# Kernel tuning notes

Hardware: AMD Instinct MI355X
Metric: run time of the kernel (lower is better)

Reference implementation:

```python
import jax, jax.numpy as jnp
import numpy as np

D = 256        # controller_lstm_size
BR = 8         # child_branch_num
UNITS = 12     # child_unit_num
TEMP = 5.0
TANHC = 1.1
MAXA = UNITS + 2   # max number of anchors
NEG = -1e9


def setup_inputs() -> dict:
    key = jax.random.key(0)
    ks = jax.random.split(key, 9)
    u = lambda k, s: jax.random.uniform(k, s, jnp.float32, -0.1, 0.1)
    # b_soft: zeros with first two entries = 10, excluded from uniform init
    b_soft = jnp.zeros((BR,), jnp.float32).at[:2].set(10.0)
    return {
        "encoder": u(ks[0], (BR + 1, D)),   # nn.Embedding(branch_num+1, D)
        "W_ih": u(ks[1], (4 * D, D)),       # LSTMCell weight_ih (i,f,g,o)
        "W_hh": u(ks[2], (4 * D, D)),
        "b_ih": u(ks[3], (4 * D,)),
        "b_hh": u(ks[4], (4 * D,)),
        "w_soft": u(ks[5], (BR, D)),
        "b_soft": b_soft,
        "w_attn_1": u(ks[6], (D, D)),
        "w_attn_2": u(ks[7], (D, D)),
        "v_attn": u(ks[8], (D,)),
    }


def _sample(key, logits):
    """Categorical sample + NLL(cross_entropy) + entropy term (batch-1)."""
    idx = jax.random.categorical(key, jax.lax.stop_gradient(logits))
    logp = jax.nn.log_softmax(logits)
    ent = -jnp.sum(jax.nn.softmax(logits) * logp)
    return idx, -logp[idx], ent


def _run_sampler(p, key, c0, h0, use_bias):
    b_no_learn = jnp.asarray([0.25, 0.25] + [-0.25] * (BR - 2), jnp.float32)

    def lstm(x, h, c):
        g = x @ p["W_ih"].T + p["b_ih"] + h @ p["W_hh"].T + p["b_hh"]
        i, f, gc, o = jnp.split(g, 4, axis=-1)
        c2 = jax.nn.sigmoid(f) * c + jax.nn.sigmoid(i) * jnp.tanh(gc)
        return jax.nn.sigmoid(o) * jnp.tanh(c2), c2

    anchors = jnp.zeros((MAXA, D), jnp.float32)
    anchors_w1 = jnp.zeros((MAXA, D), jnp.float32)
    h, c = h0, c0
    x = p["encoder"][0]
    for i in range(2):  # two seed units, anchors stay zero
        h, c = lstm(x, h, c)
        anchors_w1 = anchors_w1.at[i].set(p["w_attn_1"] @ h)

    def step(carry, unit_id):
        h, c, x, anchors, anchors_w1, key, lp, ent = carry
        mask = jnp.arange(MAXA) < unit_id
        idxs, ops = [], []
        for _ in range(2):  # sample two input indices via attention
            h, c = lstm(x, h, c)
            q = jnp.tanh(anchors_w1 + p["w_attn_2"] @ h)     # [MAXA, D]
            logits = q @ p["v_attn"]                          # [MAXA]
            logits = TANHC * jnp.tanh(logits / TEMP)
            logits = jnp.where(mask, logits, NEG)
            key, sub = jax.random.split(key)
            idx, nll, e = _sample(sub, logits)
            lp = lp + nll
            ent = ent + jax.lax.stop_gradient(e)
            x = anchors[idx]
            idxs.append(idx)
        for _ in range(2):  # sample two ops
            h, c = lstm(x, h, c)
            logits = p["w_soft"] @ h + p["b_soft"]
            logits = TANHC * jnp.tanh(logits / TEMP)
            if use_bias:
                logits = logits + b_no_learn
            key, sub = jax.random.split(key)
            op, nll, e = _sample(sub, logits)
            lp = lp + nll
            ent = ent + jax.lax.stop_gradient(e)
            x = p["encoder"][op + 1]
            ops.append(op)
        h, c = lstm(x, h, c)  # final step adds a new anchor
        anchors = anchors.at[unit_id].set(h)
        anchors_w1 = anchors_w1.at[unit_id].set(p["w_attn_1"] @ h)
        x = p["encoder"][0]
        out = jnp.stack([idxs[0], ops[0], idxs[1], ops[1]])  # [idx1,op1,idx2,op2]
        return (h, c, x, anchors, anchors_w1, key, lp, ent), out

    z = jnp.float32(0.0)
    init = (h, c, x, anchors, anchors_w1, key, z, z)
    (h, c, *_rest, lp, ent), arcs = jax.lax.scan(
        step, init, jnp.arange(2, UNITS + 2))
    return arcs.reshape(-1), ent, lp, c, h


def reference(encoder, W_ih, W_hh, b_ih, b_hh, w_soft, b_soft,
              w_attn_1, w_attn_2, v_attn):
    p = {"encoder": encoder, "W_ih": W_ih, "W_hh": W_hh, "b_ih": b_ih,
         "b_hh": b_hh, "w_soft": w_soft, "b_soft": b_soft,
         "w_attn_1": w_attn_1, "w_attn_2": w_attn_2, "v_attn": v_attn}
    k1, k2 = jax.random.split(jax.random.key(123))
    z = jnp.zeros((D,), jnp.float32)
    arc1, e1, l1, c, h = _run_sampler(p, k1, z, z, use_bias=True)
    arc2, e2, l2, _, _ = _run_sampler(p, k2, c, h, use_bias=False)
    return arc1, arc2, l1 + l2, e1 + e2
```

## Files before the change

### kernel.cpp

```cpp
#include <hip/hip_runtime.h>
#include <cstdint>

#define D     256
#define NB    32
#define TPB   256
#define HS    8
#define NROW  32
#define MAXA  14
#define UNITS 12
#define NEGV  (-1e9f)

__device__ unsigned long long g_Hq[D];
__device__ unsigned long long g_PartQ[NB*16];

__global__ void init_kernel() {
  int i = threadIdx.x;
  if (i < D) g_Hq[i] = 0ull;
  if (i < NB * 16) g_PartQ[i] = 0ull;
}

__device__ __forceinline__ void qstore(unsigned long long* p, unsigned gen,
                                       float v) {
  unsigned long long q =
      ((unsigned long long)gen << 32) | (unsigned long long)__float_as_uint(v);
  __hip_atomic_store(p, q, __ATOMIC_RELAXED, __HIP_MEMORY_SCOPE_AGENT);
}

__device__ __forceinline__ float qpoll(unsigned long long* p, unsigned gen) {
  unsigned long long q;
  long spins = 0;
  for (;;) {
    q = __hip_atomic_load(p, __ATOMIC_RELAXED, __HIP_MEMORY_SCOPE_AGENT);
    if ((unsigned)(q >> 32) == gen) break;
    __builtin_amdgcn_s_sleep(2);
    if (++spins > 50000000L) break;
  }
  return __uint_as_float((unsigned)q);
}

__device__ __forceinline__ uint32_t rotl32(uint32_t v, uint32_t n) {
  return (v << n) | (v >> (32u - n));
}

__device__ uint2 tf2x32(uint2 k, uint32_t x0, uint32_t x1) {
  uint32_t ks0 = k.x, ks1 = k.y, ks2 = 0x1BD11BDAu ^ ks0 ^ ks1;
  x0 += ks0; x1 += ks1;
#define TF4(a,b,c,d) \
  x0 += x1; x1 = rotl32(x1,(a)); x1 ^= x0; \
  x0 += x1; x1 = rotl32(x1,(b)); x1 ^= x0; \
  x0 += x1; x1 = rotl32(x1,(c)); x1 ^= x0; \
  x0 += x1; x1 = rotl32(x1,(d)); x1 ^= x0;
  TF4(13,15,26,6)  x0 += ks1; x1 += ks2 + 1u;
  TF4(17,29,16,24) x0 += ks2; x1 += ks0 + 2u;
  TF4(13,15,26,6)  x0 += ks0; x1 += ks1 + 3u;
  TF4(17,29,16,24) x0 += ks1; x1 += ks2 + 4u;
  TF4(13,15,26,6)  x0 += ks2; x1 += ks0 + 5u;
#undef TF4
  return make_uint2(x0, x1);
}

__device__ __forceinline__ float gumbelf(uint32_t bits) {
  float f = __uint_as_float((bits >> 9) | 0x3f800000u) - 1.0f;
  const float tiny = 1.17549435082228751e-38f;
  float u = fmaxf(tiny, f);
  return -logf(-logf(u));
}

__device__ __forceinline__ float sigm(float x) {
  return 0.5f + 0.5f * tanhf(0.5f * x);
}

__global__ void __launch_bounds__(TPB) ENAScontroller_21706764714567_kernel(
    const float* __restrict__ enc,   const float* __restrict__ Wih,
    const float* __restrict__ Whh,   const float* __restrict__ bih,
    const float* __restrict__ bhh,   const float* __restrict__ wsoft,
    const float* __restrict__ bsoft, const float* __restrict__ wa1,
    const float* __restrict__ wa2,   const float* __restrict__ vattn,
    float* __restrict__ out)
{
  const int b    = blockIdx.x;
  const int t    = threadIdx.x;
  const int lane = t & 63;
  const int wv_  = t >> 6;

  unsigned hgen = 0;
  unsigned pgen = 0;

  __shared__ float4 sWhh4[64 * NROW];
  __shared__ float4 sWa1p[64 * HS];
  __shared__ float4 sWa2p[64 * HS];
  __shared__ __align__(16) float s_h[D];
  __shared__ float s_part[TPB];
  __shared__ float s_pp[NB * 16];
  __shared__ float s_eW[9][NROW];
  __shared__ float s_aW[MAXA][NROW];
  __shared__ float s_aw1[MAXA][HS];
  __shared__ float s_t2[HS];
  __shared__ float s_vs[HS];
  __shared__ float s_c[HS];
  __shared__ float s_bc[NROW];
  __shared__ float s_bsoft[HS];
  __shared__ float s_log[16];
  __shared__ float s_z[16];
  __shared__ uint2 s_pair[2];
  __shared__ uint2 s_key;
  __shared__ int   s_sel;
  __shared__ float s_lp, s_ent;

  for (int idx = t; idx < 64 * NROW; idx += TPB) {
    int kk = idx >> 5, j = idx & 31;
    int grow = (j >> 3) * D + b * HS + (j & 7);
    sWhh4[idx] = *(const float4*)&Whh[grow * D + kk * 4];
  }
  for (int idx = t; idx < 64 * HS; idx += TPB) {
    int kk = idx >> 3, j = idx & 7;
    sWa1p[idx] = *(const float4*)&wa1[(b * HS + j) * D + kk * 4];
    sWa2p[idx] = *(const float4*)&wa2[(b * HS + j) * D + kk * 4];
  }
  if (t < NROW) {
    int grow = (t >> 3) * D + b * HS + (t & 7);
    s_bc[t] = bih[grow] + bhh[grow];
  }
  if (t < HS) {
    s_vs[t] = vattn[b * HS + t];
    s_bsoft[t] = bsoft[t];
    s_c[t] = 0.f;
  }
  s_h[t] = 0.f;
  if (t == 0) { s_lp = 0.f; s_ent = 0.f; }
  if (t < 2) s_pair[t] = tf2x32(make_uint2(0u, 123u), 0u, (uint32_t)t);
  __syncthreads();
  const uint2 key1 = s_pair[0];
  const uint2 key2 = s_pair[1];

  for (int m = 0; m < 8; ++m) {
    int j = wv_ * 8 + m;
    int grow = wv_ * D + b * HS + m;
    float4 wrow = *(const float4*)&Wih[grow * D + lane * 4];
    for (int r = 0; r < 9; ++r) {
      float4 ev = *(const float4*)&enc[r * D + lane * 4];
      float x = wrow.x * ev.x + wrow.y * ev.y + wrow.z * ev.z + wrow.w * ev.w;
      #pragma unroll
      for (int s = 32; s; s >>= 1) x += __shfl_xor(x, s);
      if (lane == 0) s_eW[r][j] = x;
    }
  }
  __syncthreads();

  auto LSTM = [&](const float* xd) {
    {
      int j = t & 31, p = t >> 5;
      const float4* hp = (const float4*)s_h;
      float acc = 0.f;
      #pragma unroll
      for (int q = 0; q < 8; ++q) {
        int kk = p * 8 + q;
        float4 wvv = sWhh4[kk * 32 + j];
        float4 hv  = hp[kk];
        acc += wvv.x * hv.x + wvv.y * hv.y + wvv.z * hv.z + wvv.w * hv.w;
      }
      s_part[t] = acc;
    }
    __syncthreads();
    ++hgen;
    if (t < HS) {
      float gg[4];
      #pragma unroll
      for (int q = 0; q < 4; ++q) {
        int j = q * 8 + t;
        float s = s_bc[j] + xd[j];
        #pragma unroll
        for (int p = 0; p < 8; ++p) s += s_part[p * 32 + j];
        gg[q] = s;
      }
      float c2 = sigm(gg[1]) * s_c[t] + sigm(gg[0]) * tanhf(gg[2]);
      float hn = sigm(gg[3]) * tanhf(c2);
      s_c[t] = c2;
      qstore(&g_Hq[b * HS + t], hgen, hn);
    }
    float hv = qpoll(&g_Hq[t], hgen);
    s_h[t] = hv;
    __syncthreads();
  };

  auto DOT8 = [&](const float4* M, float* dst) {
    if (t < 64) {
      int j = t & 7, p = t >> 3;
      const float4* hp = (const float4*)s_h;
      float acc = 0.f;
      #pragma unroll
      for (int q = 0; q < 8; ++q) {
        int kk = p * 8 + q;
        float4 m4 = M[kk * 8 + j];
        float4 hv = hp[kk];
        acc += m4.x * hv.x + m4.y * hv.y + m4.z * hv.z + m4.w * hv.w;
      }
      s_part[t] = acc;
    }
    __syncthreads();
    if (t < 8) {
      float s = 0.f;
      #pragma unroll
      for (int p = 0; p < 8; ++p) s += s_part[p * 8 + t];
      dst[t] = s;
    }
    __syncthreads();
  };

  auto AWC = [&](int slot) {
    const float4* hp = (const float4*)s_h;
    for (int m = 0; m < 8; ++m) {
      int j = wv_ * 8 + m;
      int grow = wv_ * D + b * HS + m;
      float4 wrow = *(const float4*)&Wih[grow * D + lane * 4];
      float4 hv = hp[lane];
      float x = wrow.x * hv.x + wrow.y * hv.y + wrow.z * hv.z + wrow.w * hv.w;
      #pragma unroll
      for (int s = 32; s; s >>= 1) x += __shfl_xor(x, s);
      if (lane == 0) s_aW[slot][j] = x;
    }
    __syncthreads();
  };

  auto ATTN = [&]() {
    DOT8(sWa2p, s_t2);
    ++pgen;
    if (t < MAXA) {
      float pa = 0.f;
      #pragma unroll
      for (int d2 = 0; d2 < HS; ++d2)
        pa += tanhf(s_aw1[t][d2] + s_t2[d2]) * s_vs[d2];
      qstore(&g_PartQ[b * 16 + t], pgen, pa);
    }
    #pragma unroll
    for (int slot = t; slot < NB * 16; slot += TPB) {
      if ((slot & 15) < MAXA) s_pp[slot] = qpoll(&g_PartQ[slot], pgen);
    }
    __syncthreads();
  };

  auto ALOGITS = [&](int u) {
    if (t < MAXA) {
      float l = 0.f;
      #pragma unroll
      for (int bb = 0; bb < NB; ++bb) l += s_pp[bb * 16 + t];
      l = 1.1f * tanhf(l / 5.0f);
      s_log[t] = (t < u) ? l : NEGV;
    }
    __syncthreads();
  };

  auto OLOGITS = [&](bool useBias) {
    if (t < 64) {
      int j = t & 7, p = t >> 3;
      const float4* hp = (const float4*)s_h;
      float acc = 0.f;
      #pragma unroll
      for (int q = 0; q < 8; ++q) {
        int kk = p * 8 + q;
        float4 m4 = *(const float4*)&wsoft[j * D + kk * 4];
        float4 hv = hp[kk];
        acc += m4.x * hv.x + m4.y * hv.y + m4.z * hv.z + m4.w * hv.w;
      }
      s_part[t] = acc;
    }
    __syncthreads();
    if (t < 8) {
      float s = 0.f;
      #pragma unroll
      for (int p = 0; p < 8; ++p) s += s_part[p * 8 + t];
      float l = s + s_bsoft[t];
      l = 1.1f * tanhf(l / 5.0f);
      if (useBias) l += (t < 2 ? 0.25f : -0.25f);
      s_log[t] = l;
    }
    __syncthreads();
  };

  auto SAMPLE = [&](int N) -> int {
    if (t < 2) s_pair[t] = tf2x32(s_key, 0u, (uint32_t)t);
    __syncthreads();
    uint2 sub = s_pair[1];
    if (t == 0) s_key = s_pair[0];
    if (t < N) {
      uint2 e = tf2x32(sub, 0u, (uint32_t)t);
      s_z[t] = s_log[t] + gumbelf(e.x ^ e.y);
    }
    __syncthreads();
    if (t == 0) {
      int bi = 0; float bz = s_z[0];
      for (int a = 1; a < N; ++a) if (s_z[a] > bz) { bz = s_z[a]; bi = a; }
      float m = s_log[0];
      for (int a = 1; a < N; ++a) m = fmaxf(m, s_log[a]);
      float ssum = 0.f, sdl = 0.f;
      for (int a = 0; a < N; ++a) {
        float d2 = s_log[a] - m;
        float e2 = expf(d2);
        ssum += e2; sdl += e2 * d2;
      }
      float ls = logf(ssum);
      s_lp  += -(s_log[bi] - m - ls);
      s_ent += ls - sdl / ssum;
      s_sel = bi;
    }
    __syncthreads();
    return s_sel;
  };

  for (int smp = 0; smp < 2; ++smp) {
    for (int idx = t; idx < MAXA * NROW; idx += TPB) (&s_aW[0][0])[idx]  = 0.f;
    for (int idx = t; idx < MAXA * HS;   idx += TPB) (&s_aw1[0][0])[idx] = 0.f;
    if (t == 0) s_key = (smp == 0) ? key1 : key2;
    __syncthreads();

    for (int sd = 0; sd < 2; ++sd) {
      if (sd == 1) DOT8(sWa1p, s_aw1[0]);
      LSTM(s_eW[0]);
    }

    bool useBias = (smp == 0);
    for (int u = 2; u < 2 + UNITS; ++u) {
      DOT8(sWa1p, s_aw1[u - 1]);
      if (u > 2) AWC(u - 1);
      LSTM(s_eW[0]);

      ATTN(); ALOGITS(u);
      int i1 = SAMPLE(MAXA);
      LSTM(s_aW[i1]);

      ATTN(); ALOGITS(u);
      int i2 = SAMPLE(MAXA);
      LSTM(s_aW[i2]);

      OLOGITS(useBias);
      int o1 = SAMPLE(8);
      LSTM(s_eW[o1 + 1]);

      OLOGITS(useBias);
      int o2 = SAMPLE(8);
      LSTM(s_eW[o2 + 1]);

      if (b == 0 && t == 0) {
        int base = smp * 48 + (u - 2) * 4;
        out[base + 0] = (float)i1;
        out[base + 1] = (float)o1;
        out[base + 2] = (float)i2;
        out[base + 3] = (float)o2;
      }
    }
  }
  if (b == 0 && t == 0) {
    out[96] = s_lp;
    out[97] = s_ent;
  }
}

extern "C" __attribute__((visibility("default")))
void kernel_launch(void* const* d_in, const int* in_sizes, int n_in,
                   void* d_out, int out_size, void* d_ws, size_t ws_size,
                   hipStream_t stream) {
  const float* enc   = (const float*)d_in[0];
  const float* Wih   = (const float*)d_in[1];
  const float* Whh   = (const float*)d_in[2];
  const float* bih   = (const float*)d_in[3];
  const float* bhh   = (const float*)d_in[4];
  const float* wsoft = (const float*)d_in[5];
  const float* bsoft = (const float*)d_in[6];
  const float* wa1   = (const float*)d_in[7];
  const float* wa2   = (const float*)d_in[8];
  const float* vattn = (const float*)d_in[9];
  float* out = (float*)d_out;

  init_kernel<<<dim3(1), dim3(512), 0, stream>>>();
  ENAScontroller_21706764714567_kernel<<<dim3(NB), dim3(TPB), 0, stream>>>(
      enc, Wih, Whh, bih, bhh, wsoft, bsoft, wa1, wa2, vattn, out);
}
```

Measured before the change: 622.1 us.

## Compute attention redundantly per block to drop cross-block partial exchange

Every block now computes the full 256-wide w_attn_1/w_attn_2 matvecs and the attention logits itself, reading the weights from global memory. This removes the second inter-block polling exchange (g_PartQ) on each attention step. The LSTM is split into pre/post halves so the w_attn_1 anchor matvec overlaps the wait for the h broadcast, and g_Hq is double-buffered by generation parity. The cost is redundant global-memory matvec work in every block, plus a shorter sleep and a lower timeout in the poll loop.

```diff
diff --git a/kernel.cpp b/kernel.cpp
--- a/kernel.cpp
+++ b/kernel.cpp
@@ -10,13 +10,11 @@
 #define UNITS 12
 #define NEGV  (-1e9f)
 
-__device__ unsigned long long g_Hq[D];
-__device__ unsigned long long g_PartQ[NB*16];
+__device__ unsigned long long g_Hq[2 * D];
 
 __global__ void init_kernel() {
   int i = threadIdx.x;
-  if (i < D) g_Hq[i] = 0ull;
-  if (i < NB * 16) g_PartQ[i] = 0ull;
+  if (i < 2 * D) g_Hq[i] = 0ull;
 }
 
 __device__ __forceinline__ void qstore(unsigned long long* p, unsigned gen,
@@ -32,8 +30,8 @@
   for (;;) {
     q = __hip_atomic_load(p, __ATOMIC_RELAXED, __HIP_MEMORY_SCOPE_AGENT);
     if ((unsigned)(q >> 32) == gen) break;
-    __builtin_amdgcn_s_sleep(2);
-    if (++spins > 50000000L) break;
+    __builtin_amdgcn_s_sleep(1);
+    if (++spins > 20000000L) break;
   }
   return __uint_as_float((unsigned)q);
 }
@@ -84,22 +82,19 @@
   const int wv_  = t >> 6;
 
   unsigned hgen = 0;
-  unsigned pgen = 0;
 
   __shared__ float4 sWhh4[64 * NROW];
-  __shared__ float4 sWa1p[64 * HS];
-  __shared__ float4 sWa2p[64 * HS];
   __shared__ __align__(16) float s_h[D];
   __shared__ float s_part[TPB];
-  __shared__ float s_pp[NB * 16];
   __shared__ float s_eW[9][NROW];
   __shared__ float s_aW[MAXA][NROW];
-  __shared__ float s_aw1[MAXA][HS];
-  __shared__ float s_t2[HS];
-  __shared__ float s_vs[HS];
+  __shared__ float s_aw1[MAXA][D];
+  __shared__ float s_t2f[D];
+  __shared__ float s_v[D];
+  __shared__ float s_red2[MAXA][32];
   __shared__ float s_c[HS];
   __shared__ float s_bc[NROW];
-  __shared__ float s_bsoft[HS];
+  __shared__ float s_bsoft[8];
   __shared__ float s_log[16];
   __shared__ float s_z[16];
   __shared__ uint2 s_pair[2];
@@ -112,20 +107,13 @@
     int grow = (j >> 3) * D + b * HS + (j & 7);
     sWhh4[idx] = *(const float4*)&Whh[grow * D + kk * 4];
   }
-  for (int idx = t; idx < 64 * HS; idx += TPB) {
-    int kk = idx >> 3, j = idx & 7;
-    sWa1p[idx] = *(const float4*)&wa1[(b * HS + j) * D + kk * 4];
-    sWa2p[idx] = *(const float4*)&wa2[(b * HS + j) * D + kk * 4];
-  }
   if (t < NROW) {
     int grow = (t >> 3) * D + b * HS + (t & 7);
     s_bc[t] = bih[grow] + bhh[grow];
   }
-  if (t < HS) {
-    s_vs[t] = vattn[b * HS + t];
-    s_bsoft[t] = bsoft[t];
-    s_c[t] = 0.f;
-  }
+  s_v[t] = vattn[t];
+  if (t < 8) s_bsoft[t] = bsoft[t];
+  if (t < HS) s_c[t] = 0.f;
   s_h[t] = 0.f;
   if (t == 0) { s_lp = 0.f; s_ent = 0.f; }
   if (t < 2) s_pair[t] = tf2x32(make_uint2(0u, 123u), 0u, (uint32_t)t);
@@ -147,7 +135,7 @@
   }
   __syncthreads();
 
-  auto LSTM = [&](const float* xd) {
+  auto LSTM_PRE = [&](const float* xd) {
     {
       int j = t & 31, p = t >> 5;
       const float4* hp = (const float4*)s_h;
@@ -176,34 +164,35 @@
       float c2 = sigm(gg[1]) * s_c[t] + sigm(gg[0]) * tanhf(gg[2]);
       float hn = sigm(gg[3]) * tanhf(c2);
       s_c[t] = c2;
-      qstore(&g_Hq[b * HS + t], hgen, hn);
-    }
-    float hv = qpoll(&g_Hq[t], hgen);
+      qstore(&g_Hq[(hgen & 1) * D + b * HS + t], hgen, hn);
+    }
+  };
+
+  auto LSTM_POST = [&]() {
+    __syncthreads();
+    float hv = qpoll(&g_Hq[(hgen & 1) * D + t], hgen);
     s_h[t] = hv;
     __syncthreads();
   };
 
-  auto DOT8 = [&](const float4* M, float* dst) {
-    if (t < 64) {
-      int j = t & 7, p = t >> 3;
-      const float4* hp = (const float4*)s_h;
-      float acc = 0.f;
+  auto DOTFULL = [&](const float* __restrict__ W, float* dst) {
+    const float4* W4 = (const float4*)W;
+    const float4* hp = (const float4*)s_h;
+    int j = t;
+    float acc = 0.f;
+    #pragma unroll
+    for (int p = 0; p < 8; ++p) {
+      float pp = 0.f;
       #pragma unroll
       for (int q = 0; q < 8; ++q) {
         int kk = p * 8 + q;
-        float4 m4 = M[kk * 8 + j];
+        float4 m4 = W4[j * 64 + kk];
         float4 hv = hp[kk];
-        acc += m4.x * hv.x + m4.y * hv.y + m4.z * hv.z + m4.w * hv.w;
-      }
-      s_part[t] = acc;
-    }
-    __syncthreads();
-    if (t < 8) {
-      float s = 0.f;
-      #pragma unroll
-      for (int p = 0; p < 8; ++p) s += s_part[p * 8 + t];
-      dst[t] = s;
-    }
+        pp += m4.x * hv.x + m4.y * hv.y + m4.z * hv.z + m4.w * hv.w;
+      }
+      acc += pp;
+    }
+    dst[j] = acc;
     __syncthreads();
   };
 
@@ -222,19 +211,17 @@
     __syncthreads();
   };
 
-  auto ATTN = [&]() {
-    DOT8(sWa2p, s_t2);
-    ++pgen;
-    if (t < MAXA) {
+  auto ATTNL = [&]() {
+    DOTFULL(wa2, s_t2f);
+    for (int idx = t; idx < MAXA * 32; idx += TPB) {
+      int a = idx >> 5, bb = idx & 31;
       float pa = 0.f;
       #pragma unroll
-      for (int d2 = 0; d2 < HS; ++d2)
-        pa += tanhf(s_aw1[t][d2] + s_t2[d2]) * s_vs[d2];
-      qstore(&g_PartQ[b * 16 + t], pgen, pa);
-    }
-    #pragma unroll
-    for (int slot = t; slot < NB * 16; slot += TPB) {
-      if ((slot & 15) < MAXA) s_pp[slot] = qpoll(&g_PartQ[slot], pgen);
+      for (int d2 = 0; d2 < 8; ++d2) {
+        int d = bb * 8 + d2;
+        pa += tanhf(s_aw1[a][d] + s_t2f[d]) * s_v[d];
+      }
+      s_red2[a][bb] = pa;
     }
     __syncthreads();
   };
@@ -243,7 +230,7 @@
     if (t < MAXA) {
       float l = 0.f;
       #pragma unroll
-      for (int bb = 0; bb < NB; ++bb) l += s_pp[bb * 16 + t];
+      for (int bb = 0; bb < NB; ++bb) l += s_red2[t][bb];
       l = 1.1f * tanhf(l / 5.0f);
       s_log[t] = (t < u) ? l : NEGV;
     }
@@ -309,36 +296,38 @@
 
   for (int smp = 0; smp < 2; ++smp) {
     for (int idx = t; idx < MAXA * NROW; idx += TPB) (&s_aW[0][0])[idx]  = 0.f;
-    for (int idx = t; idx < MAXA * HS;   idx += TPB) (&s_aw1[0][0])[idx] = 0.f;
+    for (int idx = t; idx < MAXA * D;    idx += TPB) (&s_aw1[0][0])[idx] = 0.f;
     if (t == 0) s_key = (smp == 0) ? key1 : key2;
     __syncthreads();
 
-    for (int sd = 0; sd < 2; ++sd) {
-      if (sd == 1) DOT8(sWa1p, s_aw1[0]);
-      LSTM(s_eW[0]);
-    }
+    LSTM_PRE(s_eW[0]);
+    LSTM_POST();
+    LSTM_PRE(s_eW[0]);
+    DOTFULL(wa1, s_aw1[0]);
+    LSTM_POST();
 
     bool useBias = (smp == 0);
     for (int u = 2; u < 2 + UNITS; ++u) {
-      DOT8(sWa1p, s_aw1[u - 1]);
+      LSTM_PRE(s_eW[0]);
+      DOTFULL(wa1, s_aw1[u - 1]);
       if (u > 2) AWC(u - 1);
-      LSTM(s_eW[0]);
-
-      ATTN(); ALOGITS(u);
+      LSTM_POST();
+
+      ATTNL(); ALOGITS(u);
       int i1 = SAMPLE(MAXA);
-      LSTM(s_aW[i1]);
-
-      ATTN(); ALOGITS(u);
+      LSTM_PRE(s_aW[i1]); LSTM_POST();
+
+      ATTNL(); ALOGITS(u);
       int i2 = SAMPLE(MAXA);
-      LSTM(s_aW[i2]);
+      LSTM_PRE(s_aW[i2]); LSTM_POST();
 
       OLOGITS(useBias);
       int o1 = SAMPLE(8);
-      LSTM(s_eW[o1 + 1]);
+      LSTM_PRE(s_eW[o1 + 1]); LSTM_POST();
 
       OLOGITS(useBias);
       int o2 = SAMPLE(8);
-      LSTM(s_eW[o2 + 1]);
+      LSTM_PRE(s_eW[o2 + 1]); LSTM_POST();
 
       if (b == 0 && t == 0) {
         int base = smp * 48 + (u - 2) * 4;
```

After: 877.5 us. 1.41x slower.

## Double-buffer cross-block exchange slots and overlap LSTM h exchange with DOT8

Applied to the files above, without the earlier changes.

Splits the LSTM step into a compute/publish phase and a poll/gather phase, so the attention-key DOT8 and AWC work run while other blocks' hidden states are still arriving. The global h and attention-partial exchange buffers are double-buffered by generation parity to avoid overwrite races when blocks run ahead. Polling is now done by 64 threads each fetching several slots, and the sleep interval is shortened. This adds extra block barriers and concentrates the polling latency on fewer threads.

```diff
diff --git a/kernel.cpp b/kernel.cpp
--- a/kernel.cpp
+++ b/kernel.cpp
@@ -10,13 +10,13 @@
 #define UNITS 12
 #define NEGV  (-1e9f)
 
-__device__ unsigned long long g_Hq[D];
-__device__ unsigned long long g_PartQ[NB*16];
+__device__ unsigned long long g_Hq[2 * D];
+__device__ unsigned long long g_PartQ[2 * NB*16];
 
 __global__ void init_kernel() {
   int i = threadIdx.x;
-  if (i < D) g_Hq[i] = 0ull;
-  if (i < NB * 16) g_PartQ[i] = 0ull;
+  if (i < 2 * D) g_Hq[i] = 0ull;
+  for (int s = i; s < 2 * NB * 16; s += 1024) g_PartQ[s] = 0ull;
 }
 
 __device__ __forceinline__ void qstore(unsigned long long* p, unsigned gen,
@@ -32,8 +32,8 @@
   for (;;) {
     q = __hip_atomic_load(p, __ATOMIC_RELAXED, __HIP_MEMORY_SCOPE_AGENT);
     if ((unsigned)(q >> 32) == gen) break;
-    __builtin_amdgcn_s_sleep(2);
-    if (++spins > 50000000L) break;
+    __builtin_amdgcn_s_sleep(1);
+    if (++spins > 20000000L) break;
   }
   return __uint_as_float((unsigned)q);
 }
@@ -99,7 +99,7 @@
   __shared__ float s_vs[HS];
   __shared__ float s_c[HS];
   __shared__ float s_bc[NROW];
-  __shared__ float s_bsoft[HS];
+  __shared__ float s_bsoft[8];
   __shared__ float s_log[16];
   __shared__ float s_z[16];
   __shared__ uint2 s_pair[2];
@@ -123,9 +123,9 @@
   }
   if (t < HS) {
     s_vs[t] = vattn[b * HS + t];
-    s_bsoft[t] = bsoft[t];
     s_c[t] = 0.f;
   }
+  if (t < 8) s_bsoft[t] = bsoft[t];
   s_h[t] = 0.f;
   if (t == 0) { s_lp = 0.f; s_ent = 0.f; }
   if (t < 2) s_pair[t] = tf2x32(make_uint2(0u, 123u), 0u, (uint32_t)t);
@@ -147,7 +147,7 @@
   }
   __syncthreads();
 
-  auto LSTM = [&](const float* xd) {
+  auto LSTM_PRE = [&](const float* xd) {
     {
       int j = t & 31, p = t >> 5;
       const float4* hp = (const float4*)s_h;
@@ -176,10 +176,20 @@
       float c2 = sigm(gg[1]) * s_c[t] + sigm(gg[0]) * tanhf(gg[2]);
       float hn = sigm(gg[3]) * tanhf(c2);
       s_c[t] = c2;
-      qstore(&g_Hq[b * HS + t], hgen, hn);
-    }
-    float hv = qpoll(&g_Hq[t], hgen);
-    s_h[t] = hv;
+      qstore(&g_Hq[(hgen & 1) * D + b * HS + t], hgen, hn);
+    }
+  };
+
+  auto LSTM_POST = [&]() {
+    __syncthreads();
+    if (t < 64) {
+      unsigned long long* base2 = &g_Hq[(hgen & 1) * D];
+      #pragma unroll
+      for (int k = 0; k < 4; ++k) {
+        int slot = t * 4 + k;
+        s_h[slot] = qpoll(&base2[slot], hgen);
+      }
+    }
     __syncthreads();
   };
 
@@ -230,11 +240,12 @@
       #pragma unroll
       for (int d2 = 0; d2 < HS; ++d2)
         pa += tanhf(s_aw1[t][d2] + s_t2[d2]) * s_vs[d2];
-      qstore(&g_PartQ[b * 16 + t], pgen, pa);
-    }
-    #pragma unroll
-    for (int slot = t; slot < NB * 16; slot += TPB) {
-      if ((slot & 15) < MAXA) s_pp[slot] = qpoll(&g_PartQ[slot], pgen);
+      qstore(&g_PartQ[(pgen & 1) * (NB * 16) + b * 16 + t], pgen, pa);
+    }
+    if (t < 64) {
+      unsigned long long* base2 = &g_PartQ[(pgen & 1) * (NB * 16)];
+      for (int s = t; s < NB * 16; s += 64)
+        if ((s & 15) < MAXA) s_pp[s] = qpoll(&base2[s], pgen);
     }
     __syncthreads();
   };
@@ -313,32 +324,34 @@
     if (t == 0) s_key = (smp == 0) ? key1 : key2;
     __syncthreads();
 
-    for (int sd = 0; sd < 2; ++sd) {
-      if (sd == 1) DOT8(sWa1p, s_aw1[0]);
-      LSTM(s_eW[0]);
-    }
+    LSTM_PRE(s_eW[0]);
+    LSTM_POST();
+    LSTM_PRE(s_eW[0]);
+    DOT8(sWa1p, s_aw1[0]);
+    LSTM_POST();
 
     bool useBias = (smp == 0);
     for (int u = 2; u < 2 + UNITS; ++u) {
+      LSTM_PRE(s_eW[0]);
       DOT8(sWa1p, s_aw1[u - 1]);
       if (u > 2) AWC(u - 1);
-      LSTM(s_eW[0]);
+      LSTM_POST();
 
       ATTN(); ALOGITS(u);
       int i1 = SAMPLE(MAXA);
-      LSTM(s_aW[i1]);
+      LSTM_PRE(s_aW[i1]); LSTM_POST();
 
       ATTN(); ALOGITS(u);
       int i2 = SAMPLE(MAXA);
-      LSTM(s_aW[i2]);
+      LSTM_PRE(s_aW[i2]); LSTM_POST();
 
       OLOGITS(useBias);
       int o1 = SAMPLE(8);
-      LSTM(s_eW[o1 + 1]);
+      LSTM_PRE(s_eW[o1 + 1]); LSTM_POST();
 
       OLOGITS(useBias);
       int o2 = SAMPLE(8);
-      LSTM(s_eW[o2 + 1]);
+      LSTM_PRE(s_eW[o2 + 1]); LSTM_POST();
 
       if (b == 0 && t == 0) {
         int base = smp * 48 + (u - 2) * 4;
@@ -371,7 +384,7 @@
   const float* vattn = (const float*)d_in[9];
   float* out = (float*)d_out;
 
-  init_kernel<<<dim3(1), dim3(512), 0, stream>>>();
+  init_kernel<<<dim3(1), dim3(1024), 0, stream>>>();
   ENAScontroller_21706764714567_kernel<<<dim3(NB), dim3(TPB), 0, stream>>>(
       enc, Wih, Whh, bih, bhh, wsoft, bsoft, wa1, wa2, vattn, out);
 }
```

Result: slower. 727.2 us (+16.9%).
